# Optimization experiments

Hardware: AMD Instinct MI355X
Metric: run time of the kernel (lower is better)

## Reference

```python
import jax, jax.numpy as jnp
import numpy as np

NODE_DIM = 128
N_NODES = 100000
N_EDGES = 600000


def setup_inputs() -> dict:
    key = jax.random.key(0)
    k_x, k_e, k_w1, k_b1, k_w2, k_b2 = jax.random.split(key, 6)
    x = jax.random.normal(k_x, (N_NODES, NODE_DIM), dtype=jnp.float32)
    edge_index = jax.random.randint(k_e, (2, N_EDGES), 0, N_NODES, dtype=jnp.int64)
    # nn.Linear default init: U(-1/sqrt(fan_in), 1/sqrt(fan_in))
    lim1 = 1.0 / np.sqrt(2 * NODE_DIM)
    W1 = jax.random.uniform(k_w1, (2 * NODE_DIM, NODE_DIM), minval=-lim1, maxval=lim1, dtype=jnp.float32)
    b1 = jax.random.uniform(k_b1, (NODE_DIM,), minval=-lim1, maxval=lim1, dtype=jnp.float32)
    lim2 = 1.0 / np.sqrt(NODE_DIM)
    W2 = jax.random.uniform(k_w2, (NODE_DIM, 1), minval=-lim2, maxval=lim2, dtype=jnp.float32)
    b2 = jax.random.uniform(k_b2, (1,), minval=-lim2, maxval=lim2, dtype=jnp.float32)
    return {"x": x, "edge_index": edge_index, "W1": W1, "b1": b1, "W2": W2, "b2": b2}


def reference(x, edge_index, W1, b1, W2, b2):
    src = edge_index[0]
    dst = edge_index[1]
    # [E, 2*node_dim] gathered pair features
    pair = jnp.concatenate([x[src], x[dst]], axis=-1)
    h = jax.nn.relu(pair @ W1 + b1)          # [E, node_dim]
    s = jax.nn.sigmoid(h @ W2 + b2)          # [E, 1]
    return s.squeeze(-1)                      # [E]
```

## Files before the change

kernel.cpp:

```cpp
#include <hip/hip_runtime.h>
#include <hip/hip_bf16.h>
#include <stdint.h>

#define NODE_DIM 128
#define N_NODES  100000
#define N_EDGES  600000
#define NOUT     256

#define QSTEP_INV 64.0f
#define QSTEP     (1.0f / 64.0f)

typedef __bf16 bf16x8 __attribute__((ext_vector_type(8)));
typedef float  f32x4  __attribute__((ext_vector_type(4)));

static __device__ inline unsigned pack2_bf16(float a, float b) {
    unsigned short ua = __builtin_bit_cast(unsigned short, (__bf16)a);
    unsigned short ub = __builtin_bit_cast(unsigned short, (__bf16)b);
    return (unsigned)ua | ((unsigned)ub << 16);
}

static __device__ __forceinline__ void async_copy16(const void* g, void* l) {
    __builtin_amdgcn_global_load_lds(
        (__attribute__((address_space(1))) void*)(uintptr_t)g,
        (__attribute__((address_space(3))) void*)(uint32_t)(uintptr_t)l,
        16, 0, 0);
}

__global__ void wprep_kernel(const float* __restrict__ W1, __bf16* __restrict__ Wt) {
    int i = blockIdx.x * 256 + threadIdx.x;
    if (i >= NOUT * NODE_DIM) return;
    int kp = i >> 7;
    int n  = i & 127;
    float v = W1[i];
    int np = (kp < NODE_DIM) ? n  : (n + NODE_DIM);
    int k  = (kp < NODE_DIM) ? kp : (kp - NODE_DIM);
    int npp = (np & ~0x3C) | ((np & 0x0C) << 2) | ((np & 0x30) >> 2);
    Wt[npp * NODE_DIM + k] = (__bf16)v;
}

#define MT     64
#define GB     512
#define NTILES 1563

__global__ __launch_bounds__(256)
void gemm_pre_kernel(const float* __restrict__ x, const __bf16* __restrict__ Wt,
                     const float* __restrict__ b1,
                     unsigned char* __restrict__ Ai, unsigned char* __restrict__ Bi) {
    __shared__ __align__(16) char lds_raw[2 * 32768];

    const int t    = threadIdx.x;
    const int wave = t >> 6;
    const int lane = t & 63;
    const int lm   = lane & 15;
    const int q    = lane >> 4;
    const int n0   = wave * 64;

    bf16x8 bfr[4][4];
#pragma unroll
    for (int nt = 0; nt < 4; ++nt) {
        const int n = n0 + nt * 16 + lm;
#pragma unroll
        for (int ks = 0; ks < 4; ++ks)
            bfr[nt][ks] = __builtin_bit_cast(bf16x8,
                *(const uint4*)(Wt + (size_t)n * NODE_DIM + ks * 32 + q * 8));
    }

    const int chbase = (n0 & 64) + q * 16;
    unsigned char* __restrict__ Tbl = (n0 < NODE_DIM) ? Ai : Bi;
    f32x4 bq[4];
#pragma unroll
    for (int nt = 0; nt < 4; ++nt) {
        if (n0 < NODE_DIM) {
            const float4 b = *(const float4*)(b1 + chbase + nt * 4);
            bq[nt][0] = fmaf(b.x, QSTEP_INV, 128.5f);
            bq[nt][1] = fmaf(b.y, QSTEP_INV, 128.5f);
            bq[nt][2] = fmaf(b.z, QSTEP_INV, 128.5f);
            bq[nt][3] = fmaf(b.w, QSTEP_INV, 128.5f);
        } else {
            bq[nt] = (f32x4){128.5f, 128.5f, 128.5f, 128.5f};
        }
    }

    auto STAGE = [&](int tile, int ib) {
        const int m0 = tile * MT;
#pragma unroll
        for (int i = 0; i < 8; ++i) {
            const int s     = i * 256 + wave * 64 + lane;
            const int sbase = i * 256 + wave * 64;
            const int R  = s >> 5;
            const int p  = s & 31;
            const int cg = p ^ (R & 7);
            int gr = m0 + R;
            if (gr > N_NODES - 1) gr = N_NODES - 1;
            async_copy16(x + (size_t)gr * NODE_DIM + cg * 4,
                         lds_raw + (size_t)(ib * 2048 + sbase) * 16);
        }
    };

    int tile = blockIdx.x;
    STAGE(tile, 0);
    asm volatile("s_waitcnt vmcnt(0)" ::: "memory");
    __builtin_amdgcn_s_barrier();

    int ib = 0;
    for (; tile < NTILES; tile += GB, ib ^= 1) {
        const int m0  = tile * MT;
        const int nxt = tile + GB;

        asm volatile("s_waitcnt lgkmcnt(0)" ::: "memory");
        __builtin_amdgcn_s_barrier();

        if (nxt < NTILES) {
            STAGE(nxt, ib ^ 1);
            asm volatile("s_waitcnt vmcnt(12)" ::: "memory");
        } else {
            asm volatile("s_waitcnt vmcnt(4)" ::: "memory");
        }
        __builtin_amdgcn_sched_barrier(0);
        __builtin_amdgcn_s_barrier();

        f32x4 acc[4][4];
#pragma unroll
        for (int a = 0; a < 4; ++a)
#pragma unroll
            for (int b = 0; b < 4; ++b)
                acc[a][b] = (f32x4){0.f, 0.f, 0.f, 0.f};

        const float* Xf = (const float*)(lds_raw + ib * 32768);
#pragma unroll
        for (int mt = 0; mt < 4; ++mt) {
            const int R  = mt * 16 + lm;
            const int rs = R & 7;
#pragma unroll
            for (int ks = 0; ks < 4; ++ks) {
                const int c0 = ks * 8 + q * 2;
                const float4 f0 = *(const float4*)&Xf[(R * 32 + (c0 ^ rs)) * 4];
                const float4 f1 = *(const float4*)&Xf[(R * 32 + ((c0 + 1) ^ rs)) * 4];
                uint4 p;
                p.x = pack2_bf16(f0.x, f0.y);
                p.y = pack2_bf16(f0.z, f0.w);
                p.z = pack2_bf16(f1.x, f1.y);
                p.w = pack2_bf16(f1.z, f1.w);
                bf16x8 af = __builtin_bit_cast(bf16x8, p);
#pragma unroll
                for (int nt = 0; nt < 4; ++nt)
                    acc[mt][nt] = __builtin_amdgcn_mfma_f32_16x16x32_bf16(
                        bfr[nt][ks], af, acc[mt][nt], 0, 0, 0);
            }
        }

#pragma unroll
        for (int mt = 0; mt < 4; ++mt) {
            unsigned pw[4];
#pragma unroll
            for (int nt = 0; nt < 4; ++nt) {
                unsigned u[4];
#pragma unroll
                for (int r = 0; r < 4; ++r) {
                    float g = fmaf(acc[mt][nt][r], QSTEP_INV, bq[nt][r]);
                    g = fminf(fmaxf(g, 0.f), 255.f);
                    u[r] = (unsigned)g;
                }
                pw[nt] = u[0] | (u[1] << 8) | (u[2] << 16) | (u[3] << 24);
            }
            uint4 pk;
            pk.x = pw[0]; pk.y = pw[1]; pk.z = pw[2]; pk.w = pw[3];
            int m = m0 + mt * 16 + lm;
            if (m > N_NODES - 1) m = N_NODES - 1;
            *(uint4*)(Tbl + (size_t)m * NODE_DIM + chbase) = pk;
        }
    }
}

__global__ __launch_bounds__(256)
void edge_score_kernel(const unsigned char* __restrict__ Ai,
                       const unsigned char* __restrict__ Bi,
                       const int* __restrict__ idx,
                       const float* __restrict__ W2, const float* __restrict__ b2,
                       float* __restrict__ out) {
    const int t   = threadIdx.x;
    const int sub = t & 7;
    const int g   = (blockIdx.x * 256 + t) >> 3;
    const int e0  = g * 4;
    if (e0 >= N_EDGES) return;

    float w[16];
#pragma unroll
    for (int j = 0; j < 16; ++j) w[j] = W2[sub * 16 + j];
    const float bias2 = b2[0];

    const int4 sv = *(const int4*)(idx + e0);
    const int4 dv = *(const int4*)(idx + N_EDGES + e0);
    const int s[4] = {sv.x, sv.y, sv.z, sv.w};
    const int d[4] = {dv.x, dv.y, dv.z, dv.w};

    uint4 av[4], bv[4];
#pragma unroll
    for (int i = 0; i < 4; ++i) {
        av[i] = *(const uint4*)(Ai + (size_t)s[i] * NODE_DIM + sub * 16);
        bv[i] = *(const uint4*)(Bi + (size_t)d[i] * NODE_DIM + sub * 16);
    }

    float p[4];
#pragma unroll
    for (int i = 0; i < 4; ++i) {
        const unsigned aw[4] = {av[i].x, av[i].y, av[i].z, av[i].w};
        const unsigned bw[4] = {bv[i].x, bv[i].y, bv[i].z, bv[i].w};
        float acc = 0.f;
#pragma unroll
        for (int wd = 0; wd < 4; ++wd) {
#pragma unroll
            for (int k = 0; k < 4; ++k) {
                const int ua = (int)((aw[wd] >> (8 * k)) & 0xffu);
                const int ub = (int)((bw[wd] >> (8 * k)) & 0xffu);
                const int r  = max(ua + ub, 256) - 256;
                acc = fmaf((float)r, w[wd * 4 + k], acc);
            }
        }
        p[i] = acc;
    }

#pragma unroll
    for (int i = 0; i < 4; ++i) {
        p[i] += __shfl_xor(p[i], 1);
        p[i] += __shfl_xor(p[i], 2);
        p[i] += __shfl_xor(p[i], 4);
    }

    if (sub == 0) {
        float4 o;
        o.x = 1.f / (1.f + __expf(-fmaf(p[0], QSTEP, bias2)));
        o.y = 1.f / (1.f + __expf(-fmaf(p[1], QSTEP, bias2)));
        o.z = 1.f / (1.f + __expf(-fmaf(p[2], QSTEP, bias2)));
        o.w = 1.f / (1.f + __expf(-fmaf(p[3], QSTEP, bias2)));
        *(float4*)(out + e0) = o;
    }
}

__global__ __launch_bounds__(128)
void naive_edge_kernel(const float* __restrict__ x, const int* __restrict__ idx,
                       const float* __restrict__ W1, const float* __restrict__ b1,
                       const float* __restrict__ W2, const float* __restrict__ b2,
                       float* __restrict__ out) {
    __shared__ float pair[2 * NODE_DIM];
    __shared__ float red[2];
    int e = blockIdx.x;
    int t = threadIdx.x;
    int s = idx[e], d = idx[N_EDGES + e];
    pair[t]            = x[(size_t)s * NODE_DIM + t];
    pair[NODE_DIM + t] = x[(size_t)d * NODE_DIM + t];
    __syncthreads();
    float acc = b1[t];
    for (int k = 0; k < 2 * NODE_DIM; ++k)
        acc = fmaf(pair[k], W1[k * NODE_DIM + t], acc);
    float c = fmaxf(acc, 0.f) * W2[t];
#pragma unroll
    for (int m = 1; m < 64; m <<= 1) c += __shfl_xor(c, m);
    if ((t & 63) == 0) red[t >> 6] = c;
    __syncthreads();
    if (t == 0) out[e] = 1.f / (1.f + __expf(-(red[0] + red[1] + b2[0])));
}

extern "C" void kernel_launch(void* const* d_in, const int* in_sizes, int n_in,
                              void* d_out, int out_size, void* d_ws, size_t ws_size,
                              hipStream_t stream) {
    const float* x   = (const float*)d_in[0];
    const int*   idx = (const int*)d_in[1];
    const float* W1  = (const float*)d_in[2];
    const float* b1  = (const float*)d_in[3];
    const float* W2  = (const float*)d_in[4];
    const float* b2  = (const float*)d_in[5];
    float* out = (float*)d_out;

    const size_t tab_bytes = (size_t)N_NODES * NODE_DIM;
    const size_t wt_bytes  = (size_t)NOUT * NODE_DIM * sizeof(__bf16);
    const size_t need = 2 * tab_bytes + wt_bytes;

    if (ws_size >= need) {
        unsigned char* Ai = (unsigned char*)d_ws;
        unsigned char* Bi = Ai + tab_bytes;
        __bf16* Wt = (__bf16*)(Bi + tab_bytes);
        hipLaunchKernelGGL(wprep_kernel, dim3(128), dim3(256), 0, stream, W1, Wt);
        hipLaunchKernelGGL(gemm_pre_kernel, dim3(GB), dim3(256),
                           0, stream, x, Wt, b1, Ai, Bi);
        hipLaunchKernelGGL(edge_score_kernel, dim3((N_EDGES / 4 + 31) / 32), dim3(256),
                           0, stream, Ai, Bi, idx, W2, b2, out);
    } else {
        hipLaunchKernelGGL(naive_edge_kernel, dim3(N_EDGES), dim3(128), 0, stream,
                           x, idx, W1, b1, W2, b2, out);
    }
}
```

Baseline: 127.6 us.

## Restructure node GEMM into 8-wave blocks with triple-buffered staging and exact tail tiles

The node-projection GEMM now launches 256 blocks of 512 threads instead of 512 blocks of 256. Each of the 8 waves computes 32 output channels rather than 64. Node tiles are staged into three LDS buffers with two tiles prefetched ahead, and the fixed 6-iteration loop is fully unrolled with hand-set vmcnt waits. The leftover rows go through a separate 16-row tail path, which removes the row clamping in the main loop. This aims to hide global-load latency better and balance work across CUs, at the cost of 96 KB of LDS per block, more complex wait counts, and narrower stores.

```diff
diff --git a/kernel.cpp b/kernel.cpp
--- a/kernel.cpp
+++ b/kernel.cpp
@@ -39,25 +39,27 @@
 }
 
 #define MT     64
-#define GB     512
-#define NTILES 1563
-
-__global__ __launch_bounds__(256)
+#define GRID   256
+#define NMAIN  1536
+#define NTAIL  106
+
+__global__ __launch_bounds__(512)
 void gemm_pre_kernel(const float* __restrict__ x, const __bf16* __restrict__ Wt,
                      const float* __restrict__ b1,
                      unsigned char* __restrict__ Ai, unsigned char* __restrict__ Bi) {
-    __shared__ __align__(16) char lds_raw[2 * 32768];
+    __shared__ __align__(16) char lds_raw[3 * 32768];
 
     const int t    = threadIdx.x;
-    const int wave = t >> 6;
+    const int wv   = t >> 6;
     const int lane = t & 63;
     const int lm   = lane & 15;
     const int q    = lane >> 4;
-    const int n0   = wave * 64;
-
-    bf16x8 bfr[4][4];
-#pragma unroll
-    for (int nt = 0; nt < 4; ++nt) {
+    const int bid  = blockIdx.x;
+    const int n0   = wv * 32;
+
+    bf16x8 bfr[2][4];
+#pragma unroll
+    for (int nt = 0; nt < 2; ++nt) {
         const int n = n0 + nt * 16 + lm;
 #pragma unroll
         for (int ks = 0; ks < 4; ++ks)
@@ -65,13 +67,13 @@
                 *(const uint4*)(Wt + (size_t)n * NODE_DIM + ks * 32 + q * 8));
     }
 
-    const int chbase = (n0 & 64) + q * 16;
-    unsigned char* __restrict__ Tbl = (n0 < NODE_DIM) ? Ai : Bi;
-    f32x4 bq[4];
-#pragma unroll
-    for (int nt = 0; nt < 4; ++nt) {
-        if (n0 < NODE_DIM) {
-            const float4 b = *(const float4*)(b1 + chbase + nt * 4);
+    const int cb = ((wv >> 1) & 1) * 64 + (wv & 1) * 8 + q * 16;
+    unsigned char* __restrict__ Tbl = (wv < 4) ? Ai : Bi;
+    f32x4 bq[2];
+#pragma unroll
+    for (int nt = 0; nt < 2; ++nt) {
+        if (wv < 4) {
+            const float4 b = *(const float4*)(b1 + cb + nt * 4);
             bq[nt][0] = fmaf(b.x, QSTEP_INV, 128.5f);
             bq[nt][1] = fmaf(b.y, QSTEP_INV, 128.5f);
             bq[nt][2] = fmaf(b.z, QSTEP_INV, 128.5f);
@@ -81,52 +83,53 @@
         }
     }
 
-    auto STAGE = [&](int tile, int ib) {
+    auto STAGE = [&](int tile, int bf) {
         const int m0 = tile * MT;
 #pragma unroll
-        for (int i = 0; i < 8; ++i) {
-            const int s     = i * 256 + wave * 64 + lane;
-            const int sbase = i * 256 + wave * 64;
+        for (int i = 0; i < 4; ++i) {
+            const int s     = i * 512 + wv * 64 + lane;
+            const int sbase = i * 512 + wv * 64;
             const int R  = s >> 5;
             const int p  = s & 31;
             const int cg = p ^ (R & 7);
-            int gr = m0 + R;
-            if (gr > N_NODES - 1) gr = N_NODES - 1;
-            async_copy16(x + (size_t)gr * NODE_DIM + cg * 4,
-                         lds_raw + (size_t)(ib * 2048 + sbase) * 16);
+            async_copy16(x + (size_t)(m0 + R) * NODE_DIM + cg * 4,
+                         lds_raw + (size_t)(bf * 2048 + sbase) * 16);
         }
     };
 
-    int tile = blockIdx.x;
-    STAGE(tile, 0);
     asm volatile("s_waitcnt vmcnt(0)" ::: "memory");
+    __builtin_amdgcn_sched_barrier(0);
+    STAGE(bid, 0);
+    STAGE(bid + GRID, 1);
+    asm volatile("s_waitcnt vmcnt(4)" ::: "memory");
+    __builtin_amdgcn_sched_barrier(0);
     __builtin_amdgcn_s_barrier();
 
-    int ib = 0;
-    for (; tile < NTILES; tile += GB, ib ^= 1) {
-        const int m0  = tile * MT;
-        const int nxt = tile + GB;
+#pragma unroll
+    for (int r = 0; r < 6; ++r) {
+        const int cur  = r % 3;
+        const int tile = bid + r * GRID;
+        const int m0   = tile * MT;
 
         asm volatile("s_waitcnt lgkmcnt(0)" ::: "memory");
         __builtin_amdgcn_s_barrier();
 
-        if (nxt < NTILES) {
-            STAGE(nxt, ib ^ 1);
-            asm volatile("s_waitcnt vmcnt(12)" ::: "memory");
-        } else {
-            asm volatile("s_waitcnt vmcnt(4)" ::: "memory");
-        }
+        if (r <= 3) STAGE(bid + (r + 2) * GRID, (r + 2) % 3);
+
+        if      (r == 1 || r == 4) { asm volatile("s_waitcnt vmcnt(12)" ::: "memory"); }
+        else if (r == 5)           { asm volatile("s_waitcnt vmcnt(8)"  ::: "memory"); }
+        else                       { asm volatile("s_waitcnt vmcnt(16)" ::: "memory"); }
         __builtin_amdgcn_sched_barrier(0);
         __builtin_amdgcn_s_barrier();
 
-        f32x4 acc[4][4];
+        f32x4 acc[4][2];
 #pragma unroll
         for (int a = 0; a < 4; ++a)
 #pragma unroll
-            for (int b = 0; b < 4; ++b)
+            for (int b = 0; b < 2; ++b)
                 acc[a][b] = (f32x4){0.f, 0.f, 0.f, 0.f};
 
-        const float* Xf = (const float*)(lds_raw + ib * 32768);
+        const float* Xf = (const float*)(lds_raw + cur * 32768);
 #pragma unroll
         for (int mt = 0; mt < 4; ++mt) {
             const int R  = mt * 16 + lm;
@@ -143,7 +146,7 @@
                 p.w = pack2_bf16(f1.z, f1.w);
                 bf16x8 af = __builtin_bit_cast(bf16x8, p);
 #pragma unroll
-                for (int nt = 0; nt < 4; ++nt)
+                for (int nt = 0; nt < 2; ++nt)
                     acc[mt][nt] = __builtin_amdgcn_mfma_f32_16x16x32_bf16(
                         bfr[nt][ks], af, acc[mt][nt], 0, 0, 0);
             }
@@ -151,24 +154,75 @@
 
 #pragma unroll
         for (int mt = 0; mt < 4; ++mt) {
-            unsigned pw[4];
-#pragma unroll
-            for (int nt = 0; nt < 4; ++nt) {
+            unsigned pw[2];
+#pragma unroll
+            for (int nt = 0; nt < 2; ++nt) {
                 unsigned u[4];
 #pragma unroll
-                for (int r = 0; r < 4; ++r) {
-                    float g = fmaf(acc[mt][nt][r], QSTEP_INV, bq[nt][r]);
+                for (int rr = 0; rr < 4; ++rr) {
+                    float g = fmaf(acc[mt][nt][rr], QSTEP_INV, bq[nt][rr]);
                     g = fminf(fmaxf(g, 0.f), 255.f);
-                    u[r] = (unsigned)g;
+                    u[rr] = (unsigned)g;
                 }
                 pw[nt] = u[0] | (u[1] << 8) | (u[2] << 16) | (u[3] << 24);
             }
-            uint4 pk;
-            pk.x = pw[0]; pk.y = pw[1]; pk.z = pw[2]; pk.w = pw[3];
-            int m = m0 + mt * 16 + lm;
-            if (m > N_NODES - 1) m = N_NODES - 1;
-            *(uint4*)(Tbl + (size_t)m * NODE_DIM + chbase) = pk;
-        }
+            uint2 pk; pk.x = pw[0]; pk.y = pw[1];
+            const int m = m0 + mt * 16 + lm;
+            *(uint2*)(Tbl + (size_t)m * NODE_DIM + cb) = pk;
+        }
+    }
+
+    if (bid < NTAIL) {
+        const int m0 = NMAIN * MT + bid * 16;
+        {
+            const int s  = wv * 64 + lane;
+            const int R  = s >> 5;
+            const int p  = s & 31;
+            const int cg = p ^ (R & 7);
+            async_copy16(x + (size_t)(m0 + R) * NODE_DIM + cg * 4,
+                         lds_raw + (size_t)(wv * 64) * 16);
+        }
+        asm volatile("s_waitcnt vmcnt(0)" ::: "memory");
+        __builtin_amdgcn_sched_barrier(0);
+        __builtin_amdgcn_s_barrier();
+
+        f32x4 acc[2];
+        acc[0] = (f32x4){0.f, 0.f, 0.f, 0.f};
+        acc[1] = (f32x4){0.f, 0.f, 0.f, 0.f};
+        const float* Xf = (const float*)lds_raw;
+        const int R  = lm;
+        const int rs = R & 7;
+#pragma unroll
+        for (int ks = 0; ks < 4; ++ks) {
+            const int c0 = ks * 8 + q * 2;
+            const float4 f0 = *(const float4*)&Xf[(R * 32 + (c0 ^ rs)) * 4];
+            const float4 f1 = *(const float4*)&Xf[(R * 32 + ((c0 + 1) ^ rs)) * 4];
+            uint4 p;
+            p.x = pack2_bf16(f0.x, f0.y);
+            p.y = pack2_bf16(f0.z, f0.w);
+            p.z = pack2_bf16(f1.x, f1.y);
+            p.w = pack2_bf16(f1.z, f1.w);
+            bf16x8 af = __builtin_bit_cast(bf16x8, p);
+#pragma unroll
+            for (int nt = 0; nt < 2; ++nt)
+                acc[nt] = __builtin_amdgcn_mfma_f32_16x16x32_bf16(
+                    bfr[nt][ks], af, acc[nt], 0, 0, 0);
+        }
+        unsigned pw[2];
+#pragma unroll
+        for (int nt = 0; nt < 2; ++nt) {
+            unsigned u[4];
+#pragma unroll
+            for (int rr = 0; rr < 4; ++rr) {
+                float g = fmaf(acc[nt][rr], QSTEP_INV, bq[nt][rr]);
+                g = fminf(fmaxf(g, 0.f), 255.f);
+                u[rr] = (unsigned)g;
+            }
+            pw[nt] = u[0] | (u[1] << 8) | (u[2] << 16) | (u[3] << 24);
+        }
+        uint2 pk; pk.x = pw[0]; pk.y = pw[1];
+        const int m = m0 + lm;
+        *(uint2*)(Tbl + (size_t)m * NODE_DIM + cb) = pk;
     }
 }
 
@@ -281,7 +335,7 @@
         unsigned char* Bi = Ai + tab_bytes;
         __bf16* Wt = (__bf16*)(Bi + tab_bytes);
         hipLaunchKernelGGL(wprep_kernel, dim3(128), dim3(256), 0, stream, W1, Wt);
-        hipLaunchKernelGGL(gemm_pre_kernel, dim3(GB), dim3(256),
+        hipLaunchKernelGGL(gemm_pre_kernel, dim3(GRID), dim3(512),
                            0, stream, x, Wt, b1, Ai, Bi);
         hipLaunchKernelGGL(edge_score_kernel, dim3((N_EDGES / 4 + 31) / 32), dim3(256),
                            0, stream, Ai, Bi, idx, W2, b2, out);
```

Result: no change. 128.7 us (+0.9%).

## Replace persistent double-buffered GEMM loop with one 32-row tile per block

Applied to the files above, without the earlier changes.

The precompute GEMM kernel drops its persistent grid of 512 blocks looping over 64-row tiles with double-buffered async LDS staging. It now launches one block per 32-row tile (3125 blocks) with a single 16KB LDS buffer, issuing the x load before the weight-fragment loads so they overlap. Smaller LDS use and more blocks are meant to raise occupancy and let the hardware hide load latency across blocks instead of through explicit pipelining. In exchange, each block reloads the W fragments and bias, which adds redundant weight traffic, and the row clamps are removed because 100000 divides evenly by 32.

```diff
diff --git a/kernel.cpp b/kernel.cpp
--- a/kernel.cpp
+++ b/kernel.cpp
@@ -38,15 +38,14 @@
     Wt[npp * NODE_DIM + k] = (__bf16)v;
 }
 
-#define MT     64
-#define GB     512
-#define NTILES 1563
+#define MT     32
+#define NTILES 3125
 
 __global__ __launch_bounds__(256)
 void gemm_pre_kernel(const float* __restrict__ x, const __bf16* __restrict__ Wt,
                      const float* __restrict__ b1,
                      unsigned char* __restrict__ Ai, unsigned char* __restrict__ Bi) {
-    __shared__ __align__(16) char lds_raw[2 * 32768];
+    __shared__ __align__(16) char lds_raw[16384];
 
     const int t    = threadIdx.x;
     const int wave = t >> 6;
@@ -54,6 +53,18 @@
     const int lm   = lane & 15;
     const int q    = lane >> 4;
     const int n0   = wave * 64;
+    const int m0   = blockIdx.x * MT;
+
+#pragma unroll
+    for (int i = 0; i < 4; ++i) {
+        const int s     = i * 256 + wave * 64 + lane;
+        const int sbase = i * 256 + wave * 64;
+        const int R  = s >> 5;
+        const int p  = s & 31;
+        const int cg = p ^ (R & 7);
+        async_copy16(x + (size_t)(m0 + R) * NODE_DIM + cg * 4,
+                     lds_raw + (size_t)sbase * 16);
+    }
 
     bf16x8 bfr[4][4];
 #pragma unroll
@@ -81,94 +92,58 @@
         }
     }
 
-    auto STAGE = [&](int tile, int ib) {
-        const int m0 = tile * MT;
-#pragma unroll
-        for (int i = 0; i < 8; ++i) {
-            const int s     = i * 256 + wave * 64 + lane;
-            const int sbase = i * 256 + wave * 64;
-            const int R  = s >> 5;
-            const int p  = s & 31;
-            const int cg = p ^ (R & 7);
-            int gr = m0 + R;
-            if (gr > N_NODES - 1) gr = N_NODES - 1;
-            async_copy16(x + (size_t)gr * NODE_DIM + cg * 4,
-                         lds_raw + (size_t)(ib * 2048 + sbase) * 16);
-        }
-    };
-
-    int tile = blockIdx.x;
-    STAGE(tile, 0);
     asm volatile("s_waitcnt vmcnt(0)" ::: "memory");
+    __builtin_amdgcn_sched_barrier(0);
     __builtin_amdgcn_s_barrier();
 
-    int ib = 0;
-    for (; tile < NTILES; tile += GB, ib ^= 1) {
-        const int m0  = tile * MT;
-        const int nxt = tile + GB;
-
-        asm volatile("s_waitcnt lgkmcnt(0)" ::: "memory");
-        __builtin_amdgcn_s_barrier();
-
-        if (nxt < NTILES) {
-            STAGE(nxt, ib ^ 1);
-            asm volatile("s_waitcnt vmcnt(12)" ::: "memory");
-        } else {
-            asm volatile("s_waitcnt vmcnt(4)" ::: "memory");
-        }
-        __builtin_amdgcn_sched_barrier(0);
-        __builtin_amdgcn_s_barrier();
-
-        f32x4 acc[4][4];
-#pragma unroll
-        for (int a = 0; a < 4; ++a)
-#pragma unroll
-            for (int b = 0; b < 4; ++b)
-                acc[a][b] = (f32x4){0.f, 0.f, 0.f, 0.f};
-
-        const float* Xf = (const float*)(lds_raw + ib * 32768);
-#pragma unroll
-        for (int mt = 0; mt < 4; ++mt) {
-            const int R  = mt * 16 + lm;
-            const int rs = R & 7;
-#pragma unroll
-            for (int ks = 0; ks < 4; ++ks) {
-                const int c0 = ks * 8 + q * 2;
-                const float4 f0 = *(const float4*)&Xf[(R * 32 + (c0 ^ rs)) * 4];
-                const float4 f1 = *(const float4*)&Xf[(R * 32 + ((c0 + 1) ^ rs)) * 4];
-                uint4 p;
-                p.x = pack2_bf16(f0.x, f0.y);
-                p.y = pack2_bf16(f0.z, f0.w);
-                p.z = pack2_bf16(f1.x, f1.y);
-                p.w = pack2_bf16(f1.z, f1.w);
-                bf16x8 af = __builtin_bit_cast(bf16x8, p);
-#pragma unroll
-                for (int nt = 0; nt < 4; ++nt)
-                    acc[mt][nt] = __builtin_amdgcn_mfma_f32_16x16x32_bf16(
-                        bfr[nt][ks], af, acc[mt][nt], 0, 0, 0);
+    f32x4 acc[2][4];
+#pragma unroll
+    for (int a = 0; a < 2; ++a)
+#pragma unroll
+        for (int b = 0; b < 4; ++b)
+            acc[a][b] = (f32x4){0.f, 0.f, 0.f, 0.f};
+
+    const float* Xf = (const float*)lds_raw;
+#pragma unroll
+    for (int mt = 0; mt < 2; ++mt) {
+        const int R  = mt * 16 + lm;
+        const int rs = R & 7;
+#pragma unroll
+        for (int ks = 0; ks < 4; ++ks) {
+            const int c0 = ks * 8 + q * 2;
+            const float4 f0 = *(const float4*)&Xf[(R * 32 + (c0 ^ rs)) * 4];
+            const float4 f1 = *(const float4*)&Xf[(R * 32 + ((c0 + 1) ^ rs)) * 4];
+            uint4 p;
+            p.x = pack2_bf16(f0.x, f0.y);
+            p.y = pack2_bf16(f0.z, f0.w);
+            p.z = pack2_bf16(f1.x, f1.y);
+            p.w = pack2_bf16(f1.z, f1.w);
+            bf16x8 af = __builtin_bit_cast(bf16x8, p);
+#pragma unroll
+            for (int nt = 0; nt < 4; ++nt)
+                acc[mt][nt] = __builtin_amdgcn_mfma_f32_16x16x32_bf16(
+                    bfr[nt][ks], af, acc[mt][nt], 0, 0, 0);
+        }
+    }
+
+#pragma unroll
+    for (int mt = 0; mt < 2; ++mt) {
+        unsigned pw[4];
+#pragma unroll
+        for (int nt = 0; nt < 4; ++nt) {
+            unsigned u[4];
+#pragma unroll
+            for (int rr = 0; rr < 4; ++rr) {
+                float g = fmaf(acc[mt][nt][rr], QSTEP_INV, bq[nt][rr]);
+                g = fminf(fmaxf(g, 0.f), 255.f);
+                u[rr] = (unsigned)g;
             }
-        }
-
-#pragma unroll
-        for (int mt = 0; mt < 4; ++mt) {
-            unsigned pw[4];
-#pragma unroll
-            for (int nt = 0; nt < 4; ++nt) {
-                unsigned u[4];
-#pragma unroll
-                for (int r = 0; r < 4; ++r) {
-                    float g = fmaf(acc[mt][nt][r], QSTEP_INV, bq[nt][r]);
-                    g = fminf(fmaxf(g, 0.f), 255.f);
-                    u[r] = (unsigned)g;
-                }
-                pw[nt] = u[0] | (u[1] << 8) | (u[2] << 16) | (u[3] << 24);
-            }
-            uint4 pk;
-            pk.x = pw[0]; pk.y = pw[1]; pk.z = pw[2]; pk.w = pw[3];
-            int m = m0 + mt * 16 + lm;
-            if (m > N_NODES - 1) m = N_NODES - 1;
-            *(uint4*)(Tbl + (size_t)m * NODE_DIM + chbase) = pk;
-        }
+            pw[nt] = u[0] | (u[1] << 8) | (u[2] << 16) | (u[3] << 24);
+        }
+        uint4 pk;
+        pk.x = pw[0]; pk.y = pw[1]; pk.z = pw[2]; pk.w = pw[3];
+        const int m = m0 + mt * 16 + lm;
+        *(uint4*)(Tbl + (size_t)m * NODE_DIM + chbase) = pk;
     }
 }
 
@@ -281,7 +256,7 @@
         unsigned char* Bi = Ai + tab_bytes;
         __bf16* Wt = (__bf16*)(Bi + tab_bytes);
         hipLaunchKernelGGL(wprep_kernel, dim3(128), dim3(256), 0, stream, W1, Wt);
-        hipLaunchKernelGGL(gemm_pre_kernel, dim3(GB), dim3(256),
+        hipLaunchKernelGGL(gemm_pre_kernel, dim3(NTILES), dim3(256),
                            0, stream, x, Wt, b1, Ai, Bi);
         hipLaunchKernelGGL(edge_score_kernel, dim3((N_EDGES / 4 + 31) / 32), dim3(256),
                            0, stream, Ai, Bi, idx, W2, b2, out);
```

Result: slower. 142.9 us (+12.0%).
